# Kernel tuning notes

Hardware: AMD Instinct MI355X
Metric: run time of the kernel (lower is better)

## Reference

```python
import jax, jax.numpy as jnp
import numpy as np

EMBED_DIM = 1024
NUM_HEADS = 16
HEAD_DIM = EMBED_DIM // NUM_HEADS
WINDOW = 3
N_RAND = 3
BLOCK = 64
BATCH = 2
SEQ = 2048


def _bigbird_mask(seq_len: int) -> np.ndarray:
    """Global + sliding-window + random block mask. True = attend.
    Deterministic (fixed numpy seed) stand-in for np.random.choice in the
    original; the mask is data-independent so it is a compile-time constant."""
    nb = -(-seq_len // BLOCK)  # ceil division
    mask = np.zeros((seq_len, seq_len), dtype=bool)
    g = min(BLOCK, seq_len)
    mask[:g, :] = True  # global rows
    mask[:, :g] = True  # global cols
    blk = np.arange(seq_len) // BLOCK
    # sliding window: block distance <= WINDOW (matches start/end block loop)
    mask |= np.abs(blk[:, None] - blk[None, :]) <= WINDOW
    rng = np.random.RandomState(0)
    for b in range(1, nb):
        avail = [x for x in range(1, nb) if abs(x - b) > WINDOW]
        if avail:
            sel = rng.choice(avail, size=min(N_RAND, len(avail)), replace=False)
            s0, s1 = b * BLOCK, min(seq_len, (b + 1) * BLOCK)
            for rb in sel:
                mask[s0:s1, rb * BLOCK:min(seq_len, (rb + 1) * BLOCK)] = True
    return mask


def setup_inputs() -> dict:
    key = jax.random.key(0)
    ks = jax.random.split(key, 9)
    E = EMBED_DIM
    std = E ** -0.5
    return {
        "hidden_states": jax.random.normal(ks[0], (BATCH, SEQ, E), jnp.float32),
        "wq": jax.random.normal(ks[1], (E, E), jnp.float32) * std,
        "bq": jnp.zeros((E,), jnp.float32),
        "wk": jax.random.normal(ks[2], (E, E), jnp.float32) * std,
        "bk": jnp.zeros((E,), jnp.float32),
        "wv": jax.random.normal(ks[3], (E, E), jnp.float32) * std,
        "bv": jnp.zeros((E,), jnp.float32),
        "wo": jax.random.normal(ks[4], (E, E), jnp.float32) * std,
        "bo": jnp.zeros((E,), jnp.float32),
    }


def reference(hidden_states, wq, bq, wk, bk, wv, bv, wo, bo):
    B, S, E = hidden_states.shape
    D = HEAD_DIM
    scale = D ** -0.5

    def proj(w, b):  # (B,S,E) -> (B,H,S,D)
        return (hidden_states @ w.T + b).reshape(B, S, NUM_HEADS, D).transpose(0, 2, 1, 3)

    q = proj(wq, bq)
    k = proj(wk, bk)
    v = proj(wv, bv)
    scores = jnp.einsum('bhqd,bhkd->bhqk', q, k) * scale  # dense, masked post-hoc (as in source)
    mask = jnp.asarray(_bigbird_mask(S))
    scores = jnp.where(mask[None, None, :, :], scores, -jnp.inf)
    attn = jax.nn.softmax(scores, axis=-1)
    out = jnp.einsum('bhqk,bhkd->bhqd', attn, v)
    out = out.transpose(0, 2, 1, 3).reshape(B, S, E)
    return out @ wo.T + bo
```

## Files before the change

### kernel.cpp

```cpp
#include <hip/hip_runtime.h>
#include <cstdint>
#include <math.h>


#define DEVI __device__ __forceinline__

typedef __bf16 bf16x8 __attribute__((ext_vector_type(8)));
typedef float floatx4 __attribute__((ext_vector_type(4)));
typedef unsigned short u16x8 __attribute__((ext_vector_type(8)));
typedef unsigned short u16x4 __attribute__((ext_vector_type(4)));
typedef unsigned short ushort_t;

typedef const __attribute__((address_space(1))) void* gptr_as1;
typedef __attribute__((address_space(3))) void* lptr_as3;

DEVI ushort_t f2bf(float f) {
  unsigned u = __float_as_uint(f);
  unsigned r = ((u >> 16) & 1u) + 0x7fffu;
  return (ushort_t)((u + r) >> 16);
}

DEVI void lds_load16(void* lds, const void* g) {
  __builtin_amdgcn_global_load_lds((gptr_as1)g, (lptr_as3)lds, 16, 0, 0);
}

DEVI floatx4 mfma16(bf16x8 a, bf16x8 b, floatx4 c) {
  return __builtin_amdgcn_mfma_f32_16x16x32_bf16(a, b, c, 0, 0, 0);
}

struct MTState { unsigned mt[624]; int mti; };

constexpr unsigned mt_next(MTState& s) {
  if (s.mti >= 624) {
    for (int k = 0; k < 624; ++k) {
      unsigned y = (s.mt[k] & 0x80000000u) | (s.mt[(k + 1) % 624] & 0x7fffffffu);
      unsigned v = s.mt[(k + 397) % 624] ^ (y >> 1);
      if (y & 1u) v ^= 0x9908b0dfu;
      s.mt[k] = v;
    }
    s.mti = 0;
  }
  unsigned y = s.mt[s.mti++];
  y ^= y >> 11;
  y ^= (y << 7) & 0x9d2c5680u;
  y ^= (y << 15) & 0xefc60000u;
  y ^= y >> 18;
  return y;
}

constexpr unsigned mt_interval(MTState& s, unsigned mx) {
  if (mx == 0u) return 0u;
  unsigned msk = mx;
  msk |= msk >> 1; msk |= msk >> 2; msk |= msk >> 4; msk |= msk >> 8; msk |= msk >> 16;
  unsigned v = mt_next(s) & msk;
  while (v > mx) v = mt_next(s) & msk;
  return v;
}

struct MaskPack { unsigned char list[32][32]; int cnt[32]; };

constexpr MaskPack make_pack() {
  unsigned char m[32][32] = {};
  for (int i = 0; i < 32; ++i)
    for (int j = 0; j < 32; ++j) {
      int d = i - j; if (d < 0) d = -d;
      m[i][j] = (i == 0 || j == 0 || d <= 3) ? (unsigned char)1 : (unsigned char)0;
    }
  MTState st{};
  st.mt[0] = 0u;
  for (int i = 1; i < 624; ++i)
    st.mt[i] = 1812433253u * (st.mt[i - 1] ^ (st.mt[i - 1] >> 30)) + (unsigned)i;
  st.mti = 624;
  for (int b = 1; b < 32; ++b) {
    int avail[32] = {}; int n = 0;
    for (int x = 1; x < 32; ++x) {
      int d = x - b; if (d < 0) d = -d;
      if (d > 3) avail[n++] = x;
    }
    if (n == 0) continue;
    int perm[32] = {};
    for (int i = 0; i < n; ++i) perm[i] = i;
    for (int i = n - 1; i > 0; --i) {
      unsigned j = mt_interval(st, (unsigned)i);
      int t = perm[i]; perm[i] = perm[(int)j]; perm[(int)j] = t;
    }
    int take = n < 3 ? n : 3;
    for (int s = 0; s < take; ++s) m[b][avail[perm[s]]] = 1;
  }
  MaskPack P{};
  for (int i = 0; i < 32; ++i) {
    int c = 0;
    for (int j = 0; j < 32; ++j)
      if (m[i][j]) P.list[i][c++] = (unsigned char)j;
    P.cnt[i] = c;
  }
  return P;
}

__constant__ MaskPack MP = make_pack();

__global__ __launch_bounds__(256) void cvt_all(
    const float* __restrict__ hs, const float* __restrict__ wq,
    const float* __restrict__ wk, const float* __restrict__ wv,
    const float* __restrict__ wo,
    ushort_t* __restrict__ hs_bf, ushort_t* __restrict__ wq_bf,
    ushort_t* __restrict__ wk_bf, ushort_t* __restrict__ wv_bf,
    ushort_t* __restrict__ wo_bf) {
  const int i = blockIdx.x * 256 + threadIdx.x;
  const float* s;
  ushort_t* d;
  int j;
  if (i < 1048576) {
    s = hs; d = hs_bf; j = i;
  } else {
    const int t = (i - 1048576) >> 18;
    j = (i - 1048576) & 262143;
    s = t == 0 ? wq : (t == 1 ? wk : (t == 2 ? wv : wo));
    d = t == 0 ? wq_bf : (t == 1 ? wk_bf : (t == 2 ? wv_bf : wo_bf));
  }
  const float4 f = ((const float4*)s)[j];
  u16x4 o;
  o.x = f2bf(f.x); o.y = f2bf(f.y); o.z = f2bf(f.z); o.w = f2bf(f.w);
  ((u16x4*)d)[j] = o;
}

__global__ __launch_bounds__(256) void gemm_qkv(
    const ushort_t* __restrict__ A,
    const ushort_t* __restrict__ W0, const ushort_t* __restrict__ W1, const ushort_t* __restrict__ W2,
    const float* __restrict__ b0, const float* __restrict__ b1, const float* __restrict__ b2,
    void* __restrict__ o0, void* __restrict__ o1, void* __restrict__ o2) {
  constexpr int N = 1024, K = 1024;
  __shared__ alignas(16) ushort_t As[128 * 32];
  __shared__ alignas(16) ushort_t Bs[128 * 32];
  const int z = blockIdx.z;
  const ushort_t* Bw = z == 0 ? W0 : (z == 1 ? W1 : W2);
  const float* bias = z == 0 ? b0 : (z == 1 ? b1 : b2);
  void* Cout = z == 0 ? o0 : (z == 1 ? o1 : o2);

  const int tid = threadIdx.x;
  const int w = tid >> 6, l = tid & 63, quad = l >> 4, li = l & 15;
  const int m0 = blockIdx.x * 128, n0 = blockIdx.y * 128;
  const int wm = (w >> 1) * 64, wn = (w & 1) * 64;

  const int lof0 = (w * 2 + 0) * 512 + l * 8;
  const int lof1 = (w * 2 + 1) * 512 + l * 8;
  const int rA0 = lof0 >> 5, cA0 = lof0 & 31;
  const int rA1 = lof1 >> 5, cA1 = lof1 & 31;
  const ushort_t* gA0 = A + (size_t)(m0 + rA0) * K + cA0;
  const ushort_t* gA1 = A + (size_t)(m0 + rA1) * K + cA1;
  const ushort_t* gB0 = Bw + (size_t)(n0 + rA0) * K + cA0;
  const ushort_t* gB1 = Bw + (size_t)(n0 + rA1) * K + cA1;

  const floatx4 fzero = {0.0f, 0.0f, 0.0f, 0.0f};
  floatx4 acc[4][4];
#pragma unroll
  for (int i = 0; i < 4; ++i)
#pragma unroll
    for (int j = 0; j < 4; ++j) acc[i][j] = fzero;

  for (int k0 = 0; k0 < K; k0 += 32) {
    lds_load16(As + lof0, gA0 + k0);
    lds_load16(As + lof1, gA1 + k0);
    lds_load16(Bs + lof0, gB0 + k0);
    lds_load16(Bs + lof1, gB1 + k0);
    __syncthreads();
    bf16x8 af[4], bfr[4];
#pragma unroll
    for (int mi = 0; mi < 4; ++mi)
      af[mi] = *(const bf16x8*)(As + (wm + mi * 16 + li) * 32 + quad * 8);
#pragma unroll
    for (int ni = 0; ni < 4; ++ni)
      bfr[ni] = *(const bf16x8*)(Bs + (wn + ni * 16 + li) * 32 + quad * 8);
#pragma unroll
    for (int mi = 0; mi < 4; ++mi)
#pragma unroll
      for (int ni = 0; ni < 4; ++ni)
        acc[mi][ni] = mfma16(af[mi], bfr[ni], acc[mi][ni]);
    __syncthreads();
  }

  if (z == 2) {
    ushort_t* Vt = (ushort_t*)Cout;
#pragma unroll
    for (int ni = 0; ni < 4; ++ni) {
      const int col = n0 + wn + ni * 16 + li;
      const float bv = bias[col];
      const int hh = col >> 6, dd = col & 63;
#pragma unroll
      for (int mi = 0; mi < 4; ++mi) {
        const int row0 = m0 + wm + mi * 16 + quad * 4;
        const int bb = row0 >> 11, s0 = row0 & 2047;
        u16x4 pk;
#pragma unroll
        for (int r = 0; r < 4; ++r) pk[r] = f2bf(acc[mi][ni][r] + bv);
        *(u16x4*)(Vt + (size_t)((bb * 16 + hh) * 64 + dd) * 2048 + s0) = pk;
      }
    }
  } else {
#pragma unroll
    for (int ni = 0; ni < 4; ++ni) {
      const int col = n0 + wn + ni * 16 + li;
      const float bv = bias[col];
#pragma unroll
      for (int mi = 0; mi < 4; ++mi) {
#pragma unroll
        for (int r = 0; r < 4; ++r) {
          const int row = m0 + wm + mi * 16 + quad * 4 + r;
          ((ushort_t*)Cout)[(size_t)row * N + col] = f2bf(acc[mi][ni][r] + bv);
        }
      }
    }
  }
}

__global__ __launch_bounds__(256) void gemm_o64(
    const ushort_t* __restrict__ A, const ushort_t* __restrict__ W,
    const float* __restrict__ bias, float* __restrict__ C) {
  constexpr int N = 1024, K = 1024;
  __shared__ alignas(16) ushort_t As[64 * 32];
  __shared__ alignas(16) ushort_t Bs[128 * 32];
  const int tid = threadIdx.x;
  const int w = tid >> 6, l = tid & 63, quad = l >> 4, li = l & 15;
  const int m0 = blockIdx.x * 64, n0 = blockIdx.y * 128;
  const int wm = (w >> 1) * 32, wn = (w & 1) * 64;

  const int lofA = w * 512 + l * 8;
  const int rA = lofA >> 5, cA = lofA & 31;
  const int lofB0 = (w * 2 + 0) * 512 + l * 8;
  const int lofB1 = (w * 2 + 1) * 512 + l * 8;
  const int rB0 = lofB0 >> 5, cB0 = lofB0 & 31;
  const int rB1 = lofB1 >> 5, cB1 = lofB1 & 31;
  const ushort_t* gA = A + (size_t)(m0 + rA) * K + cA;
  const ushort_t* gB0 = W + (size_t)(n0 + rB0) * K + cB0;
  const ushort_t* gB1 = W + (size_t)(n0 + rB1) * K + cB1;

  const floatx4 fzero = {0.0f, 0.0f, 0.0f, 0.0f};
  floatx4 acc[2][4];
#pragma unroll
  for (int i = 0; i < 2; ++i)
#pragma unroll
    for (int j = 0; j < 4; ++j) acc[i][j] = fzero;

  for (int k0 = 0; k0 < K; k0 += 32) {
    lds_load16(As + lofA, gA + k0);
    lds_load16(Bs + lofB0, gB0 + k0);
    lds_load16(Bs + lofB1, gB1 + k0);
    __syncthreads();
    bf16x8 af[2], bfr[4];
#pragma unroll
    for (int mi = 0; mi < 2; ++mi)
      af[mi] = *(const bf16x8*)(As + (wm + mi * 16 + li) * 32 + quad * 8);
#pragma unroll
    for (int ni = 0; ni < 4; ++ni)
      bfr[ni] = *(const bf16x8*)(Bs + (wn + ni * 16 + li) * 32 + quad * 8);
#pragma unroll
    for (int mi = 0; mi < 2; ++mi)
#pragma unroll
      for (int ni = 0; ni < 4; ++ni)
        acc[mi][ni] = mfma16(af[mi], bfr[ni], acc[mi][ni]);
    __syncthreads();
  }

#pragma unroll
  for (int ni = 0; ni < 4; ++ni) {
    const int col = n0 + wn + ni * 16 + li;
    const float bv = bias[col];
#pragma unroll
    for (int mi = 0; mi < 2; ++mi) {
#pragma unroll
      for (int r = 0; r < 4; ++r) {
        const int row = m0 + wm + mi * 16 + quad * 4 + r;
        C[(size_t)row * N + col] = acc[mi][ni][r] + bv;
      }
    }
  }
}

__global__ __launch_bounds__(256) void attn_kernel(
    const ushort_t* __restrict__ Q, const ushort_t* __restrict__ Kg,
    const ushort_t* __restrict__ Vtg, ushort_t* __restrict__ O) {
  __shared__ alignas(16) ushort_t Kls[64 * 72];
  __shared__ alignas(16) ushort_t Vls[64 * 72];
  __shared__ alignas(16) ushort_t Ps[4][16 * 72];

  const int tid = threadIdx.x;
  const int w = tid >> 6, l = tid & 63, quad = l >> 4, li = l & 15;
  const int hb = blockIdx.x, qb = blockIdx.y;
  const int h = hb & 15, b = hb >> 4;
  const size_t qoff = (size_t)b * 2048 * 1024 + (size_t)h * 64;
  const size_t vtoff = (size_t)hb * 64 * 2048;

  unsigned lw[8];
#pragma unroll
  for (int j = 0; j < 8; ++j) lw[j] = ((const unsigned*)(MP.list[qb]))[j];
  const int nact = MP.cnt[qb];
  auto roll = [&]() -> int {
    const int kb = (int)(lw[0] & 255u);
#pragma unroll
    for (int j = 0; j < 7; ++j) lw[j] = (lw[j] >> 8) | (lw[j + 1] << 24);
    lw[7] >>= 8;
    return kb;
  };

  const int qrow = qb * 64 + w * 16 + li;
  bf16x8 aq0 = *(const bf16x8*)(Q + qoff + (size_t)qrow * 1024 + quad * 8);
  bf16x8 aq1 = *(const bf16x8*)(Q + qoff + (size_t)qrow * 1024 + 32 + quad * 8);
#pragma unroll
  for (int j = 0; j < 8; ++j) {
    aq0[j] = (__bf16)((float)aq0[j] * 0.125f);
    aq1[j] = (__bf16)((float)aq1[j] * 0.125f);
  }

  const floatx4 fzero = {0.0f, 0.0f, 0.0f, 0.0f};
  floatx4 o_acc[4];
  float lp[4];
#pragma unroll
  for (int nt = 0; nt < 4; ++nt) o_acc[nt] = fzero;
#pragma unroll
  for (int r = 0; r < 4; ++r) lp[r] = 0.0f;

  const int r0 = w * 16 + (l >> 3);
  const int r1 = r0 + 8;
  const int cb = (l & 7) * 8;
  const ushort_t* kg0 = Kg + qoff + (size_t)r0 * 1024 + cb;
  const ushort_t* kg1 = Kg + qoff + (size_t)r1 * 1024 + cb;
  const ushort_t* vg0 = Vtg + vtoff + (size_t)r0 * 2048 + cb;
  const ushort_t* vg1 = Vtg + vtoff + (size_t)r1 * 2048 + cb;
  ushort_t* kd0 = Kls + r0 * 72 + cb;
  ushort_t* kd1 = Kls + r1 * 72 + cb;
  ushort_t* vd0 = Vls + r0 * 72 + cb;
  ushort_t* vd1 = Vls + r1 * 72 + cb;
  ushort_t* PsW = Ps[w];

  int kb = roll();
  {
    const u16x8 a0 = *(const u16x8*)(kg0 + (size_t)kb * 65536);
    const u16x8 a1 = *(const u16x8*)(kg1 + (size_t)kb * 65536);
    const u16x8 b0 = *(const u16x8*)(vg0 + kb * 64);
    const u16x8 b1 = *(const u16x8*)(vg1 + kb * 64);
    *(u16x8*)kd0 = a0; *(u16x8*)kd1 = a1;
    *(u16x8*)vd0 = b0; *(u16x8*)vd1 = b1;
  }

  for (int i = 0; i < nact; ++i) {
    const int kbn = (i + 1 < nact) ? roll() : 0;
    __syncthreads();

    floatx4 s[4];
#pragma unroll
    for (int nt = 0; nt < 4; ++nt) {
      const bf16x8 bk0 = *(const bf16x8*)(Kls + (nt * 16 + li) * 72 + quad * 8);
      const bf16x8 bk1 = *(const bf16x8*)(Kls + (nt * 16 + li) * 72 + 32 + quad * 8);
      s[nt] = mfma16(aq1, bk1, mfma16(aq0, bk0, fzero));
    }

#pragma unroll
    for (int nt = 0; nt < 4; ++nt)
#pragma unroll
      for (int r = 0; r < 4; ++r) {
        const float e = __expf(s[nt][r]);
        lp[r] += e;
        PsW[(quad * 4 + r) * 72 + nt * 16 + li] = f2bf(e);
      }

#pragma unroll
    for (int c = 0; c < 2; ++c) {
      const bf16x8 pa = *(const bf16x8*)(PsW + li * 72 + c * 32 + quad * 8);
#pragma unroll
      for (int nt = 0; nt < 4; ++nt) {
        const bf16x8 vb = *(const bf16x8*)(Vls + (nt * 16 + li) * 72 + c * 32 + quad * 8);
        o_acc[nt] = mfma16(pa, vb, o_acc[nt]);
      }
    }

    __syncthreads();
    if (i + 1 < nact) {
      const u16x8 a0 = *(const u16x8*)(kg0 + (size_t)kbn * 65536);
      const u16x8 a1 = *(const u16x8*)(kg1 + (size_t)kbn * 65536);
      const u16x8 b0 = *(const u16x8*)(vg0 + kbn * 64);
      const u16x8 b1 = *(const u16x8*)(vg1 + kbn * 64);
      *(u16x8*)kd0 = a0; *(u16x8*)kd1 = a1;
      *(u16x8*)vd0 = b0; *(u16x8*)vd1 = b1;
    }
  }

#pragma unroll
  for (int stp = 1; stp <= 8; stp <<= 1)
#pragma unroll
    for (int r = 0; r < 4; ++r) lp[r] += __shfl_xor(lp[r], stp);

#pragma unroll
  for (int r = 0; r < 4; ++r) {
    const float rinv = 1.0f / lp[r];
#pragma unroll
    for (int nt = 0; nt < 4; ++nt) {
      const float ov = o_acc[nt][r] * rinv;
      O[qoff + (size_t)(qb * 64 + w * 16 + quad * 4 + r) * 1024 + nt * 16 + li] = f2bf(ov);
    }
  }
}

extern "C" void kernel_launch(void* const* d_in, const int* in_sizes, int n_in,
                              void* d_out, int out_size, void* d_ws, size_t ws_size,
                              hipStream_t stream) {
  const float* hs = (const float*)d_in[0];
  const float* wq = (const float*)d_in[1];
  const float* bq = (const float*)d_in[2];
  const float* wk = (const float*)d_in[3];
  const float* bk = (const float*)d_in[4];
  const float* wv = (const float*)d_in[5];
  const float* bv = (const float*)d_in[6];
  const float* wo = (const float*)d_in[7];
  const float* bo = (const float*)d_in[8];
  float* out = (float*)d_out;

  char* ws = (char*)d_ws;
  ushort_t* hs_bf = (ushort_t*)(ws);
  ushort_t* wq_bf = (ushort_t*)(ws + (8ull << 20));
  ushort_t* wk_bf = (ushort_t*)(ws + (10ull << 20));
  ushort_t* wv_bf = (ushort_t*)(ws + (12ull << 20));
  ushort_t* wo_bf = (ushort_t*)(ws + (14ull << 20));
  ushort_t* Qb = (ushort_t*)(ws + (16ull << 20));
  ushort_t* Kb = (ushort_t*)(ws + (24ull << 20));
  ushort_t* Vt = (ushort_t*)(ws + (32ull << 20));
  ushort_t* AO = hs_bf;

  cvt_all<<<8192, 256, 0, stream>>>(hs, wq, wk, wv, wo,
                                    hs_bf, wq_bf, wk_bf, wv_bf, wo_bf);

  dim3 gq(32, 8, 3);
  gemm_qkv<<<gq, 256, 0, stream>>>(hs_bf, wq_bf, wk_bf, wv_bf, bq, bk, bv, Qb, Kb, Vt);

  dim3 ga(32, 32, 1);
  attn_kernel<<<ga, 256, 0, stream>>>(Qb, Kb, Vt, AO);

  dim3 go(64, 8, 1);
  gemm_o64<<<go, 256, 0, stream>>>(AO, wo_bf, bo, out);
}
```

Before: 195.3 us.

## Rewrite QKV GEMM as 256x256-tile pipelined kernel with swizzled LDS

Replaces the 128x128 QKV projection GEMM with a 512-thread kernel that computes 256x256 output tiles over the concatenated Q/K/V weight space. It uses double-buffered LDS staging through direct global-to-LDS loads, explicit vmcnt/lgkmcnt waits and barriers to overlap loads with MFMA work, and an XOR-swizzled LDS layout to avoid bank conflicts. It also remaps block indices for cache locality and raises MFMA priority. The aim is higher MFMA utilisation and less global traffic per FLOP. In exchange, the grid is only 192 blocks, which may not fill every CU, and the hand-placed waits are easy to get wrong.

```diff
diff --git a/kernel.cpp b/kernel.cpp
--- a/kernel.cpp
+++ b/kernel.cpp
@@ -27,6 +27,12 @@
 DEVI floatx4 mfma16(bf16x8 a, bf16x8 b, floatx4 c) {
   return __builtin_amdgcn_mfma_f32_16x16x32_bf16(a, b, c, 0, 0, 0);
 }
+
+#define BARR() do { asm volatile("" ::: "memory"); \
+                    __builtin_amdgcn_s_barrier();  \
+                    asm volatile("" ::: "memory"); } while (0)
+#define LGKM0() asm volatile("s_waitcnt lgkmcnt(0)" ::: "memory")
+#define VMC(N) asm volatile("s_waitcnt vmcnt(" #N ")" ::: "memory")
 
 struct MTState { unsigned mt[624]; int mti; };
 
@@ -124,93 +130,181 @@
   ((u16x4*)d)[j] = o;
 }
 
-__global__ __launch_bounds__(256) void gemm_qkv(
+DEVI void stage_half(ushort_t* ldsb, const ushort_t* g, int w, int l) {
+  lds_load16(ldsb + w * 1024 + l * 8, g);
+  lds_load16(ldsb + w * 1024 + 512 + l * 8, g + 8192);
+}
+
+DEVI void rdA(bf16x8 (&a)[4][2], const ushort_t* base, int wm, int li, int quad) {
+#pragma unroll
+  for (int mi = 0; mi < 4; ++mi) {
+    const int rh = wm * 64 + mi * 16 + li;
+    const int sw = rh & 7;
+#pragma unroll
+    for (int ks = 0; ks < 2; ++ks)
+      a[mi][ks] = *(const bf16x8*)(base + rh * 64 + (((ks * 4 + quad) ^ sw) << 3));
+  }
+}
+
+DEVI void rdB(bf16x8 (&b)[2][2], const ushort_t* base, int wn, int li, int quad) {
+#pragma unroll
+  for (int ni = 0; ni < 2; ++ni) {
+    const int rh = wn * 32 + ni * 16 + li;
+    const int sw = rh & 7;
+#pragma unroll
+    for (int ks = 0; ks < 2; ++ks)
+      b[ni][ks] = *(const bf16x8*)(base + rh * 64 + (((ks * 4 + quad) ^ sw) << 3));
+  }
+}
+
+DEVI void mm16(floatx4 (&c)[4][2], const bf16x8 (&a)[4][2], const bf16x8 (&b)[2][2]) {
+  __builtin_amdgcn_s_setprio(1);
+#pragma unroll
+  for (int ks = 0; ks < 2; ++ks)
+#pragma unroll
+    for (int mi = 0; mi < 4; ++mi)
+#pragma unroll
+      for (int ni = 0; ni < 2; ++ni)
+        c[mi][ni] = mfma16(a[mi][ks], b[ni][ks], c[mi][ni]);
+  __builtin_amdgcn_s_setprio(0);
+}
+
+__global__ __launch_bounds__(512, 2) void gemm_qkv_fused(
     const ushort_t* __restrict__ A,
-    const ushort_t* __restrict__ W0, const ushort_t* __restrict__ W1, const ushort_t* __restrict__ W2,
-    const float* __restrict__ b0, const float* __restrict__ b1, const float* __restrict__ b2,
-    void* __restrict__ o0, void* __restrict__ o1, void* __restrict__ o2) {
-  constexpr int N = 1024, K = 1024;
-  __shared__ alignas(16) ushort_t As[128 * 32];
-  __shared__ alignas(16) ushort_t Bs[128 * 32];
-  const int z = blockIdx.z;
-  const ushort_t* Bw = z == 0 ? W0 : (z == 1 ? W1 : W2);
-  const float* bias = z == 0 ? b0 : (z == 1 ? b1 : b2);
-  void* Cout = z == 0 ? o0 : (z == 1 ? o1 : o2);
-
+    const ushort_t* __restrict__ W0, const ushort_t* __restrict__ W1,
+    const ushort_t* __restrict__ W2,
+    const float* __restrict__ bq, const float* __restrict__ bk,
+    const float* __restrict__ bv,
+    ushort_t* __restrict__ Qo, ushort_t* __restrict__ Ko,
+    ushort_t* __restrict__ Vt) {
+  __shared__ alignas(16) ushort_t LDS[2][2][2][8192];
   const int tid = threadIdx.x;
   const int w = tid >> 6, l = tid & 63, quad = l >> 4, li = l & 15;
-  const int m0 = blockIdx.x * 128, n0 = blockIdx.y * 128;
-  const int wm = (w >> 1) * 64, wn = (w & 1) * 64;
-
-  const int lof0 = (w * 2 + 0) * 512 + l * 8;
-  const int lof1 = (w * 2 + 1) * 512 + l * 8;
-  const int rA0 = lof0 >> 5, cA0 = lof0 & 31;
-  const int rA1 = lof1 >> 5, cA1 = lof1 & 31;
-  const ushort_t* gA0 = A + (size_t)(m0 + rA0) * K + cA0;
-  const ushort_t* gA1 = A + (size_t)(m0 + rA1) * K + cA1;
-  const ushort_t* gB0 = Bw + (size_t)(n0 + rA0) * K + cA0;
-  const ushort_t* gB1 = Bw + (size_t)(n0 + rA1) * K + cA1;
-
-  const floatx4 fzero = {0.0f, 0.0f, 0.0f, 0.0f};
-  floatx4 acc[4][4];
-#pragma unroll
-  for (int i = 0; i < 4; ++i)
-#pragma unroll
-    for (int j = 0; j < 4; ++j) acc[i][j] = fzero;
-
-  for (int k0 = 0; k0 < K; k0 += 32) {
-    lds_load16(As + lof0, gA0 + k0);
-    lds_load16(As + lof1, gA1 + k0);
-    lds_load16(Bs + lof0, gB0 + k0);
-    lds_load16(Bs + lof1, gB1 + k0);
-    __syncthreads();
-    bf16x8 af[4], bfr[4];
-#pragma unroll
-    for (int mi = 0; mi < 4; ++mi)
-      af[mi] = *(const bf16x8*)(As + (wm + mi * 16 + li) * 32 + quad * 8);
-#pragma unroll
-    for (int ni = 0; ni < 4; ++ni)
-      bfr[ni] = *(const bf16x8*)(Bs + (wn + ni * 16 + li) * 32 + quad * 8);
-#pragma unroll
-    for (int mi = 0; mi < 4; ++mi)
-#pragma unroll
-      for (int ni = 0; ni < 4; ++ni)
-        acc[mi][ni] = mfma16(af[mi], bfr[ni], acc[mi][ni]);
-    __syncthreads();
-  }
-
-  if (z == 2) {
-    ushort_t* Vt = (ushort_t*)Cout;
-#pragma unroll
-    for (int ni = 0; ni < 4; ++ni) {
-      const int col = n0 + wn + ni * 16 + li;
-      const float bv = bias[col];
-      const int hh = col >> 6, dd = col & 63;
-#pragma unroll
-      for (int mi = 0; mi < 4; ++mi) {
-        const int row0 = m0 + wm + mi * 16 + quad * 4;
-        const int bb = row0 >> 11, s0 = row0 & 2047;
-        u16x4 pk;
-#pragma unroll
-        for (int r = 0; r < 4; ++r) pk[r] = f2bf(acc[mi][ni][r] + bv);
-        *(u16x4*)(Vt + (size_t)((bb * 16 + hh) * 64 + dd) * 2048 + s0) = pk;
-      }
-    }
-  } else {
-#pragma unroll
-    for (int ni = 0; ni < 4; ++ni) {
-      const int col = n0 + wn + ni * 16 + li;
-      const float bv = bias[col];
-#pragma unroll
-      for (int mi = 0; mi < 4; ++mi) {
-#pragma unroll
-        for (int r = 0; r < 4; ++r) {
-          const int row = m0 + wm + mi * 16 + quad * 4 + r;
-          ((ushort_t*)Cout)[(size_t)row * N + col] = f2bf(acc[mi][ni][r] + bv);
+  const int wm = w >> 2, wn = w & 3;
+  const int bid = blockIdx.x;
+  const int swz = (bid & 7) * 24 + (bid >> 3);
+  const int m0 = (swz / 12) << 8;
+  const int n0g = (swz % 12) << 8;
+  const int z = n0g >> 10, n0l = n0g & 1023;
+  const ushort_t* Bw = z == 0 ? W0 : (z == 1 ? W1 : W2);
+  const float* bias = z == 0 ? bq : (z == 1 ? bk : bv);
+
+  const int rst = w * 16 + (l >> 3);
+  const int cst = ((l & 7) ^ (l >> 3)) << 3;
+  const ushort_t* gA = A + (size_t)(m0 + rst) * 1024 + cst;
+  const ushort_t* gB = Bw + (size_t)(n0l + rst) * 1024 + cst;
+
+  const floatx4 fz = {0.0f, 0.0f, 0.0f, 0.0f};
+  floatx4 acc[2][2][4][2];
+#pragma unroll
+  for (int qm = 0; qm < 2; ++qm)
+#pragma unroll
+    for (int qn = 0; qn < 2; ++qn)
+#pragma unroll
+      for (int mi = 0; mi < 4; ++mi)
+#pragma unroll
+        for (int ni = 0; ni < 2; ++ni) acc[qm][qn][mi][ni] = fz;
+
+  bf16x8 a[4][2], b0[2][2], b1[2][2];
+
+  stage_half(&LDS[0][0][0][0], gA, w, l);
+  stage_half(&LDS[0][0][1][0], gA + 131072, w, l);
+  stage_half(&LDS[0][1][0][0], gB, w, l);
+  stage_half(&LDS[0][1][1][0], gB + 131072, w, l);
+  stage_half(&LDS[1][0][0][0], gA + 64, w, l);
+  stage_half(&LDS[1][1][0][0], gB + 64, w, l);
+  stage_half(&LDS[1][1][1][0], gB + 131072 + 64, w, l);
+  VMC(6);
+  BARR();
+
+#pragma unroll 1
+  for (int it = 0; it < 8; ++it) {
+    const bool pf = (it < 7);
+    const int o_cy = (2 * it + 1) * 64;
+    const int o_x = (2 * it + 2) * 64;
+    const int o_y = (2 * it + 3) * 64;
+
+    rdA(a, &LDS[0][0][0][0], wm, li, quad);
+    rdB(b0, &LDS[0][1][0][0], wn, li, quad);
+    stage_half(&LDS[1][0][1][0], gA + 131072 + o_cy, w, l);
+    BARR(); LGKM0();
+    mm16(acc[0][0], a, b0);
+    BARR();
+
+    rdB(b1, &LDS[0][1][1][0], wn, li, quad);
+    if (pf) stage_half(&LDS[0][0][0][0], gA + o_x, w, l);
+    BARR(); LGKM0();
+    mm16(acc[0][1], a, b1);
+    BARR();
+
+    rdA(a, &LDS[0][0][1][0], wm, li, quad);
+    if (pf) stage_half(&LDS[0][1][0][0], gB + o_x, w, l);
+    BARR(); LGKM0();
+    mm16(acc[1][0], a, b0);
+    BARR();
+
+    if (pf) stage_half(&LDS[0][1][1][0], gB + 131072 + o_x, w, l);
+    BARR(); LGKM0();
+    mm16(acc[1][1], a, b1);
+    if (pf) { VMC(6); } else { VMC(0); }
+    BARR();
+
+    rdA(a, &LDS[1][0][0][0], wm, li, quad);
+    rdB(b0, &LDS[1][1][0][0], wn, li, quad);
+    if (pf) stage_half(&LDS[0][0][1][0], gA + 131072 + o_x, w, l);
+    BARR(); LGKM0();
+    mm16(acc[0][0], a, b0);
+    BARR();
+
+    rdB(b1, &LDS[1][1][1][0], wn, li, quad);
+    if (pf) stage_half(&LDS[1][0][0][0], gA + o_y, w, l);
+    BARR(); LGKM0();
+    mm16(acc[0][1], a, b1);
+    BARR();
+
+    rdA(a, &LDS[1][0][1][0], wm, li, quad);
+    if (pf) stage_half(&LDS[1][1][0][0], gB + o_y, w, l);
+    BARR(); LGKM0();
+    mm16(acc[1][0], a, b0);
+    BARR();
+
+    if (pf) stage_half(&LDS[1][1][1][0], gB + 131072 + o_y, w, l);
+    BARR(); LGKM0();
+    mm16(acc[1][1], a, b1);
+    if (pf) { VMC(6); }
+    BARR();
+  }
+
+#pragma unroll
+  for (int Qm = 0; Qm < 2; ++Qm)
+#pragma unroll
+    for (int Qn = 0; Qn < 2; ++Qn)
+#pragma unroll
+      for (int ni = 0; ni < 2; ++ni) {
+        const int col = n0l + Qn * 128 + wn * 32 + ni * 16 + li;
+        const float bb_ = bias[col];
+        if (z == 2) {
+          const int hh = col >> 6, dd = col & 63;
+#pragma unroll
+          for (int mi = 0; mi < 4; ++mi) {
+            const int row0 = m0 + Qm * 128 + wm * 64 + mi * 16 + quad * 4;
+            const int bb = row0 >> 11, s0 = row0 & 2047;
+            u16x4 pk;
+#pragma unroll
+            for (int r = 0; r < 4; ++r) pk[r] = f2bf(acc[Qm][Qn][mi][ni][r] + bb_);
+            *(u16x4*)(Vt + (size_t)((bb * 16 + hh) * 64 + dd) * 2048 + s0) = pk;
+          }
+        } else {
+          ushort_t* Co = (z == 0) ? Qo : Ko;
+#pragma unroll
+          for (int mi = 0; mi < 4; ++mi)
+#pragma unroll
+            for (int r = 0; r < 4; ++r) {
+              const int row = m0 + Qm * 128 + wm * 64 + mi * 16 + quad * 4 + r;
+              Co[(size_t)row * 1024 + col] = f2bf(acc[Qm][Qn][mi][ni][r] + bb_);
+            }
         }
       }
-    }
-  }
 }
 
 __global__ __launch_bounds__(256) void gemm_o64(
@@ -428,8 +522,8 @@
   cvt_all<<<8192, 256, 0, stream>>>(hs, wq, wk, wv, wo,
                                     hs_bf, wq_bf, wk_bf, wv_bf, wo_bf);
 
-  dim3 gq(32, 8, 3);
-  gemm_qkv<<<gq, 256, 0, stream>>>(hs_bf, wq_bf, wk_bf, wv_bf, bq, bk, bv, Qb, Kb, Vt);
+  gemm_qkv_fused<<<192, 512, 0, stream>>>(hs_bf, wq_bf, wk_bf, wv_bf,
+                                          bq, bk, bv, Qb, Kb, Vt);
 
   dim3 ga(32, 32, 1);
   attn_kernel<<<ga, 256, 0, stream>>>(Qb, Kb, Vt, AO);
```

New measurement: 184.3 us. 5.6% less time.
